# Kernel tuning notes

Hardware: AMD Instinct MI355X
Metric: run time of the kernel (lower is better)

Reference implementation:

```python
import jax, jax.numpy as jnp
import numpy as np

B, S, D, E = 8, 2048, 1024, 8


def setup_inputs() -> dict:
    key = jax.random.key(0)
    k1, k2, k3, k4 = jax.random.split(key, 4)
    return {
        "x": jax.random.normal(k1, (B, S, D), dtype=jnp.float32),
        "routing_scores": jax.random.normal(k2, (B, E), dtype=jnp.float32),
        "expert_w": jax.random.normal(k3, (E, D, D), dtype=jnp.float32) / np.sqrt(D),
        "expert_b": jax.random.normal(k4, (E, D), dtype=jnp.float32),
        "k": 2,
    }


def reference(x, routing_scores, expert_w, expert_b, k):
    batch = routing_scores.shape[0]
    # top-k gating mask + renormalization scale (torch.topk + scatter_ equivalent)
    values, indices = jax.lax.top_k(routing_scores, k)              # (B, k)
    mask = jnp.zeros_like(routing_scores, dtype=bool)
    mask = mask.at[jnp.arange(batch)[:, None], indices].set(True)    # (B, E)
    scale = 1.0 / (values.sum(axis=1, keepdims=True) + 1e-8)         # (B, 1)
    masked_scores = scale * routing_scores * mask                    # (B, E)

    # dense per-expert transform: expert_e(x) = x @ W_e + b_e  -> (E, B, S, D)
    expert_out = jnp.einsum("bsd,edf->ebsf", x, expert_w) + expert_b[:, None, None, :]
    # weighted scatter-accumulate over experts (zero weight for inactive pairs)
    final_output = jnp.einsum("be,ebsf->bsf", masked_scores, expert_out)

    return final_output, mask.sum(axis=0)
```

## Files before the change

### kernel.cpp

```cpp
#include <hip/hip_runtime.h>

#define NB 8
#define NS 2048
#define ND 1024
#define NE 8

typedef unsigned short ushort_t;
typedef __attribute__((ext_vector_type(8))) short bf16x8;
typedef __attribute__((ext_vector_type(4))) float f32x4;

__device__ __forceinline__ unsigned short f2bf(float f) {
    union { float f; unsigned int u; } x; x.f = f;
    unsigned int u = x.u + 0x7fffu + ((x.u >> 16) & 1u);
    return (unsigned short)(u >> 16);
}

__device__ __forceinline__ unsigned pk2(float a, float b) {
    return (unsigned)f2bf(a) | ((unsigned)f2bf(b) << 16);
}

__device__ __forceinline__ void gload16(const void* g, void* l) {
    __builtin_amdgcn_global_load_lds(
        (const __attribute__((address_space(1))) unsigned int*)g,
        (__attribute__((address_space(3))) unsigned int*)l, 16, 0, 0);
}

__device__ __forceinline__ void coef_local(const float* __restrict__ scores,
                                           int b, int k, float* cf) {
    float s[NE];
#pragma unroll
    for (int e = 0; e < NE; ++e) s[e] = scores[b * NE + e];
    bool sel[NE];
#pragma unroll
    for (int e = 0; e < NE; ++e) sel[e] = false;
    float sum = 0.f;
    for (int j = 0; j < k; ++j) {
        int best = 0; float bv = -3.4e38f;
#pragma unroll
        for (int e = 0; e < NE; ++e)
            if (!sel[e] && s[e] > bv) { bv = s[e]; best = e; }
        sel[best] = true; sum += bv;
    }
    float scale = 1.f / (sum + 1e-8f);
#pragma unroll
    for (int e = 0; e < NE; ++e) cf[e] = sel[e] ? scale * s[e] : 0.f;
}

__global__ void prep_kernel(const float* __restrict__ scores,
                            const float* __restrict__ W,
                            const float* __restrict__ eb,
                            const int* __restrict__ kp,
                            ushort_t* __restrict__ wct,
                            float* __restrict__ bias,
                            float* __restrict__ counts) {
    __shared__ float tile[64][65];
    __shared__ int selS[NB][NE];
    int bid = blockIdx.x;
    int t = threadIdx.x;

    if (bid < 2048) {
        int b = bid >> 8;
        int f0 = (bid & 15) * 64, d0 = ((bid >> 4) & 15) * 64;
        float cf[NE];
        coef_local(scores, b, kp[0], cf);
        int lr = t >> 4;
        int lc = (t & 15) * 4;
        float4 acc[4];
#pragma unroll
        for (int it = 0; it < 4; ++it) acc[it] = make_float4(0.f, 0.f, 0.f, 0.f);
#pragma unroll
        for (int e = 0; e < NE; ++e) {
            float c = cf[e];
            if (c != 0.f) {
                const float* We = W + ((size_t)e * ND * ND);
#pragma unroll
                for (int it = 0; it < 4; ++it) {
                    int d = d0 + lr + it * 16;
                    float4 v = *(const float4*)(We + (size_t)d * ND + f0 + lc);
                    acc[it].x += c * v.x; acc[it].y += c * v.y;
                    acc[it].z += c * v.z; acc[it].w += c * v.w;
                }
            }
        }
#pragma unroll
        for (int it = 0; it < 4; ++it) {
            int r = lr + it * 16;
            tile[r][lc + 0] = acc[it].x; tile[r][lc + 1] = acc[it].y;
            tile[r][lc + 2] = acc[it].z; tile[r][lc + 3] = acc[it].w;
        }
        __syncthreads();
        int dl = t & 63;
        int frow = t >> 6;
        ushort_t* dst = wct + (size_t)b * ND * ND + (size_t)f0 * ND + d0 + dl;
#pragma unroll
        for (int it = 0; it < 16; ++it) {
            int f = frow + it * 4;
            dst[(size_t)f * ND] = f2bf(tile[dl][f]);
        }
    } else if (bid < 2080) {
        int i = bid - 2048;
        int b = i >> 2, f = (i & 3) * 256 + t;
        float cf[NE];
        coef_local(scores, b, kp[0], cf);
        float acc = 0.f;
#pragma unroll
        for (int e = 0; e < NE; ++e)
            if (cf[e] != 0.f) acc += cf[e] * eb[e * ND + f];
        bias[b * ND + f] = acc;
    } else {
        int k = kp[0];
        if (t < NB) {
            float s[NE];
#pragma unroll
            for (int e = 0; e < NE; ++e) s[e] = scores[t * NE + e];
            bool sel[NE];
#pragma unroll
            for (int e = 0; e < NE; ++e) sel[e] = false;
            for (int j = 0; j < k; ++j) {
                int best = 0; float bv = -3.4e38f;
#pragma unroll
                for (int e = 0; e < NE; ++e)
                    if (!sel[e] && s[e] > bv) { bv = s[e]; best = e; }
                sel[best] = true;
            }
#pragma unroll
            for (int e = 0; e < NE; ++e) selS[t][e] = sel[e] ? 1 : 0;
        }
        __syncthreads();
        if (t < NE) {
            int c = 0;
#pragma unroll
            for (int b = 0; b < NB; ++b) c += selS[b][t];
            counts[t] = (float)c;
        }
    }
}

__global__ __launch_bounds__(512, 4) void gemm_kernel(const float* __restrict__ x,
                                                      const ushort_t* __restrict__ wct,
                                                      const float* __restrict__ bias,
                                                      float* __restrict__ out) {
    __shared__ ushort_t ldsA[3][256 * 32];
    __shared__ ushort_t ldsB[3][128 * 32];

    int bid = blockIdx.x;
    int b = bid & 7;
    int tile = bid >> 3;
    int m0 = (tile >> 3) * 256;
    int n0 = (tile & 7) * 128;
    const ushort_t* Bt = wct + ((size_t)b * ND * ND) + (size_t)n0 * ND;

    int t = threadIdx.x, lane = t & 63, wave = t >> 6;
    int wm = wave >> 1, wn = wave & 1;
    int fr = lane & 15, fq = lane >> 4;

    int srow = t >> 2;
    int slotg = (t & 3) ^ ((srow >> 1) & 3);
    const ushort_t* sB = Bt + (size_t)srow * ND + slotg * 8;
    int ldstB = t * 8;

    int ar = t >> 1, ah = t & 1;
    const float* xA = x + ((size_t)b * NS * ND) + (size_t)(m0 + ar) * ND + ah * 16;
    int swA = (ar >> 1) & 3;
    int woff0 = ar * 32 + ((2 * ah) ^ swA) * 8;
    int woff1 = ar * 32 + ((2 * ah + 1) ^ swA) * 8;

    int swzb = (fq ^ ((fr >> 1) & 3)) * 16;
    int aoff[4], boff[4];
#pragma unroll
    for (int mi = 0; mi < 4; ++mi) aoff[mi] = (wm * 64 + mi * 16 + fr) * 64 + swzb;
#pragma unroll
    for (int nj = 0; nj < 4; ++nj) boff[nj] = (wn * 64 + nj * 16 + fr) * 64 + swzb;

    f32x4 acc[4][4];
#pragma unroll
    for (int i = 0; i < 4; ++i)
#pragma unroll
        for (int j = 0; j < 4; ++j) acc[i][j] = (f32x4){0.f, 0.f, 0.f, 0.f};

    const int NT = ND / 32;

    float4 rA0, rA1, rA2, rA3;
#define LOAD_A(kt) do { \
    const float* xp = xA + (kt) * 32; \
    rA0 = *(const float4*)(xp);      rA1 = *(const float4*)(xp + 4); \
    rA2 = *(const float4*)(xp + 8);  rA3 = *(const float4*)(xp + 12); \
} while (0)
#define CVT_WRITE(buf) do { \
    uint4 o0, o1; \
    o0.x = pk2(rA0.x, rA0.y); o0.y = pk2(rA0.z, rA0.w); \
    o0.z = pk2(rA1.x, rA1.y); o0.w = pk2(rA1.z, rA1.w); \
    o1.x = pk2(rA2.x, rA2.y); o1.y = pk2(rA2.z, rA2.w); \
    o1.z = pk2(rA3.x, rA3.y); o1.w = pk2(rA3.z, rA3.w); \
    *(uint4*)(&ldsA[buf][woff0]) = o0; \
    *(uint4*)(&ldsA[buf][woff1]) = o1; \
} while (0)

    LOAD_A(0);
    gload16(sB, &ldsB[0][ldstB]);
    gload16(sB + 32, &ldsB[1][ldstB]);
    asm volatile("s_waitcnt vmcnt(2)" ::: "memory");
    CVT_WRITE(0);
    LOAD_A(1);
    asm volatile("s_waitcnt vmcnt(5)" ::: "memory");
    asm volatile("s_waitcnt lgkmcnt(0)" ::: "memory");
    __builtin_amdgcn_s_barrier();

    for (int kt = 0; kt < NT; ++kt) {
        int cur = kt; while (cur >= 3) cur -= 3;
        const char* lA = (const char*)&ldsA[cur][0];
        const char* lB = (const char*)&ldsB[cur][0];
        int nb = cur + 1; if (nb == 3) nb = 0;
        int sq = cur + 2; if (sq >= 3) sq -= 3;

        if (kt + 2 < NT) gload16(sB + (kt + 2) * 32, &ldsB[sq][ldstB]);

        bf16x8 af[4], bf[4];
#pragma unroll
        for (int nj = 0; nj < 4; ++nj) bf[nj] = *(const bf16x8*)(lB + boff[nj]);
#pragma unroll
        for (int mi = 0; mi < 4; ++mi) af[mi] = *(const bf16x8*)(lA + aoff[mi]);
        __builtin_amdgcn_sched_barrier(0);
        asm volatile("s_waitcnt lgkmcnt(0)" ::: "memory");
        __builtin_amdgcn_sched_barrier(0);
        __builtin_amdgcn_s_setprio(1);
#pragma unroll
        for (int mi = 0; mi < 4; ++mi)
#pragma unroll
            for (int nj = 0; nj < 4; ++nj)
                acc[mi][nj] = __builtin_amdgcn_mfma_f32_16x16x32_bf16(af[mi], bf[nj], acc[mi][nj], 0, 0, 0);
        __builtin_amdgcn_s_setprio(0);
        __builtin_amdgcn_sched_barrier(0);

        if (kt + 1 < NT) {
            if (kt + 2 < NT) asm volatile("s_waitcnt vmcnt(1)" ::: "memory");
            else             asm volatile("s_waitcnt vmcnt(0)" ::: "memory");
            __builtin_amdgcn_sched_barrier(0);
            CVT_WRITE(nb);
            if (kt + 2 < NT) LOAD_A(kt + 2);
            __builtin_amdgcn_sched_barrier(0);
            asm volatile("s_waitcnt lgkmcnt(0)" ::: "memory");
            __builtin_amdgcn_s_barrier();
        }
    }

#undef LOAD_A
#undef CVT_WRITE

    const float* bs = bias + b * ND;
    float* O = out + ((size_t)b * NS * ND);
#pragma unroll
    for (int mi = 0; mi < 4; ++mi) {
        int row = m0 + wm * 64 + mi * 16 + fq * 4;
#pragma unroll
        for (int nj = 0; nj < 4; ++nj) {
            int col = n0 + wn * 64 + nj * 16 + fr;
            float bv = bs[col];
            f32x4 v = acc[mi][nj];
#pragma unroll
            for (int r = 0; r < 4; ++r)
                O[(size_t)(row + r) * ND + col] = v[r] + bv;
        }
    }
}

extern "C" void kernel_launch(void* const* d_in, const int* in_sizes, int n_in,
                              void* d_out, int out_size, void* d_ws, size_t ws_size,
                              hipStream_t stream) {
    const float* x      = (const float*)d_in[0];
    const float* scores = (const float*)d_in[1];
    const float* Wx     = (const float*)d_in[2];
    const float* eb     = (const float*)d_in[3];
    const int*   kp     = (const int*)d_in[4];
    float* out = (float*)d_out;
    char* ws = (char*)d_ws;

    float*    bias  = (float*)(ws + 1024);
    ushort_t* wct   = (ushort_t*)(ws + 65536);
    float*    counts = out + (size_t)NB * NS * ND;

    prep_kernel<<<2081, 256, 0, stream>>>(scores, Wx, eb, kp, wct, bias, counts);
    gemm_kernel<<<512, 512, 0, stream>>>(x, wct, bias, out);
}
```

Measured before the change: 74.31 us.

## Split GEMM into producer/consumer waves with smaller 128x128 tiles

After: 126.2 us. 69.9% more time.

```diff
diff --git a/kernel.cpp b/kernel.cpp
--- a/kernel.cpp
+++ b/kernel.cpp
@@ -136,131 +136,133 @@
     }
 }
 
-__global__ __launch_bounds__(512, 4) void gemm_kernel(const float* __restrict__ x,
+__global__ __launch_bounds__(384, 4) void gemm_kernel(const float* __restrict__ x,
                                                       const ushort_t* __restrict__ wct,
                                                       const float* __restrict__ bias,
                                                       float* __restrict__ out) {
-    __shared__ ushort_t ldsA[3][256 * 32];
-    __shared__ ushort_t ldsB[3][128 * 32];
+    __shared__ ushort_t lA[2][128 * 32];
+    __shared__ ushort_t lB[2][128 * 32];
 
     int bid = blockIdx.x;
     int b = bid & 7;
     int tile = bid >> 3;
-    int m0 = (tile >> 3) * 256;
+    int m0 = (tile >> 3) * 128;
     int n0 = (tile & 7) * 128;
-    const ushort_t* Bt = wct + ((size_t)b * ND * ND) + (size_t)n0 * ND;
 
     int t = threadIdx.x, lane = t & 63, wave = t >> 6;
-    int wm = wave >> 1, wn = wave & 1;
-    int fr = lane & 15, fq = lane >> 4;
-
-    int srow = t >> 2;
-    int slotg = (t & 3) ^ ((srow >> 1) & 3);
-    const ushort_t* sB = Bt + (size_t)srow * ND + slotg * 8;
-    int ldstB = t * 8;
-
-    int ar = t >> 1, ah = t & 1;
-    const float* xA = x + ((size_t)b * NS * ND) + (size_t)(m0 + ar) * ND + ah * 16;
-    int swA = (ar >> 1) & 3;
-    int woff0 = ar * 32 + ((2 * ah) ^ swA) * 8;
-    int woff1 = ar * 32 + ((2 * ah + 1) ^ swA) * 8;
-
-    int swzb = (fq ^ ((fr >> 1) & 3)) * 16;
-    int aoff[4], boff[4];
-#pragma unroll
-    for (int mi = 0; mi < 4; ++mi) aoff[mi] = (wm * 64 + mi * 16 + fr) * 64 + swzb;
-#pragma unroll
-    for (int nj = 0; nj < 4; ++nj) boff[nj] = (wn * 64 + nj * 16 + fr) * 64 + swzb;
-
-    f32x4 acc[4][4];
-#pragma unroll
-    for (int i = 0; i < 4; ++i)
-#pragma unroll
-        for (int j = 0; j < 4; ++j) acc[i][j] = (f32x4){0.f, 0.f, 0.f, 0.f};
-
     const int NT = ND / 32;
 
-    float4 rA0, rA1, rA2, rA3;
-#define LOAD_A(kt) do { \
-    const float* xp = xA + (kt) * 32; \
-    rA0 = *(const float4*)(xp);      rA1 = *(const float4*)(xp + 4); \
-    rA2 = *(const float4*)(xp + 8);  rA3 = *(const float4*)(xp + 12); \
+    if (wave < 4) {
+        int wm = wave >> 1, wn = wave & 1;
+        int fr = lane & 15, fq = lane >> 4;
+        int swzb = (fq ^ ((fr >> 1) & 3)) * 16;
+        int aoff[4], boff[4];
+#pragma unroll
+        for (int mi = 0; mi < 4; ++mi) aoff[mi] = (wm * 64 + mi * 16 + fr) * 64 + swzb;
+#pragma unroll
+        for (int nj = 0; nj < 4; ++nj) boff[nj] = (wn * 64 + nj * 16 + fr) * 64 + swzb;
+
+        f32x4 acc[4][4];
+#pragma unroll
+        for (int i = 0; i < 4; ++i)
+#pragma unroll
+            for (int j = 0; j < 4; ++j) acc[i][j] = (f32x4){0.f, 0.f, 0.f, 0.f};
+
+        asm volatile("" ::: "memory");
+        __builtin_amdgcn_s_barrier();
+        asm volatile("" ::: "memory");
+
+        for (int kt = 0; kt < NT; ++kt) {
+            const char* pA = (const char*)&lA[kt & 1][0];
+            const char* pB = (const char*)&lB[kt & 1][0];
+            bf16x8 af[4], bf[4];
+#pragma unroll
+            for (int nj = 0; nj < 4; ++nj) bf[nj] = *(const bf16x8*)(pB + boff[nj]);
+#pragma unroll
+            for (int mi = 0; mi < 4; ++mi) af[mi] = *(const bf16x8*)(pA + aoff[mi]);
+            __builtin_amdgcn_s_setprio(1);
+#pragma unroll
+            for (int mi = 0; mi < 4; ++mi)
+#pragma unroll
+                for (int nj = 0; nj < 4; ++nj)
+                    acc[mi][nj] = __builtin_amdgcn_mfma_f32_16x16x32_bf16(af[mi], bf[nj], acc[mi][nj], 0, 0, 0);
+            __builtin_amdgcn_s_setprio(0);
+            if (kt + 1 < NT) {
+                asm volatile("s_waitcnt lgkmcnt(0)" ::: "memory");
+                __builtin_amdgcn_s_barrier();
+                asm volatile("" ::: "memory");
+            }
+        }
+
+        const float* bs = bias + b * ND;
+        float* O = out + ((size_t)b * NS * ND);
+#pragma unroll
+        for (int mi = 0; mi < 4; ++mi) {
+            int row = m0 + wm * 64 + mi * 16 + fq * 4;
+#pragma unroll
+            for (int nj = 0; nj < 4; ++nj) {
+                int col = n0 + wn * 64 + nj * 16 + fr;
+                float bv = bs[col];
+                f32x4 v = acc[mi][nj];
+#pragma unroll
+                for (int r = 0; r < 4; ++r)
+                    O[(size_t)(row + r) * ND + col] = v[r] + bv;
+            }
+        }
+    } else {
+        int p = t - 256;
+        int pw = wave - 4;
+        const float* xA = x + (size_t)b * NS * ND + (size_t)(m0 + p) * ND;
+        int wsw = (p >> 1) & 3;
+        int brow = pw * 64 + (lane >> 2);
+        int slotB = (lane & 3) ^ ((lane >> 3) & 3);
+        const ushort_t* sB = wct + (size_t)b * ND * ND + (size_t)(n0 + brow) * ND + slotB * 8;
+
+        float4 r[8];
+#define LOADA(kt) do { \
+    const float4* xp = (const float4*)(xA + (kt) * 32); \
+    _Pragma("unroll") \
+    for (int j = 0; j < 8; ++j) r[j] = xp[j]; \
 } while (0)
-#define CVT_WRITE(buf) do { \
-    uint4 o0, o1; \
-    o0.x = pk2(rA0.x, rA0.y); o0.y = pk2(rA0.z, rA0.w); \
-    o0.z = pk2(rA1.x, rA1.y); o0.w = pk2(rA1.z, rA1.w); \
-    o1.x = pk2(rA2.x, rA2.y); o1.y = pk2(rA2.z, rA2.w); \
-    o1.z = pk2(rA3.x, rA3.y); o1.w = pk2(rA3.z, rA3.w); \
-    *(uint4*)(&ldsA[buf][woff0]) = o0; \
-    *(uint4*)(&ldsA[buf][woff1]) = o1; \
+#define GLB(kt, buf) do { \
+    _Pragma("unroll") \
+    for (int i = 0; i < 4; ++i) \
+        gload16(sB + (kt) * 32 + (size_t)(i * 16) * ND, &lB[buf][(pw * 64 + i * 16) * 32]); \
 } while (0)
-
-    LOAD_A(0);
-    gload16(sB, &ldsB[0][ldstB]);
-    gload16(sB + 32, &ldsB[1][ldstB]);
-    asm volatile("s_waitcnt vmcnt(2)" ::: "memory");
-    CVT_WRITE(0);
-    LOAD_A(1);
-    asm volatile("s_waitcnt vmcnt(5)" ::: "memory");
-    asm volatile("s_waitcnt lgkmcnt(0)" ::: "memory");
-    __builtin_amdgcn_s_barrier();
-
-    for (int kt = 0; kt < NT; ++kt) {
-        int cur = kt; while (cur >= 3) cur -= 3;
-        const char* lA = (const char*)&ldsA[cur][0];
-        const char* lB = (const char*)&ldsB[cur][0];
-        int nb = cur + 1; if (nb == 3) nb = 0;
-        int sq = cur + 2; if (sq >= 3) sq -= 3;
-
-        if (kt + 2 < NT) gload16(sB + (kt + 2) * 32, &ldsB[sq][ldstB]);
-
-        bf16x8 af[4], bf[4];
-#pragma unroll
-        for (int nj = 0; nj < 4; ++nj) bf[nj] = *(const bf16x8*)(lB + boff[nj]);
-#pragma unroll
-        for (int mi = 0; mi < 4; ++mi) af[mi] = *(const bf16x8*)(lA + aoff[mi]);
-        __builtin_amdgcn_sched_barrier(0);
+#define CVTW(buf) do { \
+    _Pragma("unroll") \
+    for (int j = 0; j < 4; ++j) { \
+        uint4 o; \
+        o.x = pk2(r[2 * j].x, r[2 * j].y);         o.y = pk2(r[2 * j].z, r[2 * j].w); \
+        o.z = pk2(r[2 * j + 1].x, r[2 * j + 1].y); o.w = pk2(r[2 * j + 1].z, r[2 * j + 1].w); \
+        *(uint4*)(&lA[buf][p * 32 + ((j ^ wsw) * 8)]) = o; \
+    } \
+} while (0)
+
+        LOADA(0);
+        GLB(0, 0);
+        asm volatile("s_waitcnt vmcnt(4)" ::: "memory");
+        CVTW(0);
+        asm volatile("s_waitcnt vmcnt(0)" ::: "memory");
         asm volatile("s_waitcnt lgkmcnt(0)" ::: "memory");
-        __builtin_amdgcn_sched_barrier(0);
-        __builtin_amdgcn_s_setprio(1);
-#pragma unroll
-        for (int mi = 0; mi < 4; ++mi)
-#pragma unroll
-            for (int nj = 0; nj < 4; ++nj)
-                acc[mi][nj] = __builtin_amdgcn_mfma_f32_16x16x32_bf16(af[mi], bf[nj], acc[mi][nj], 0, 0, 0);
-        __builtin_amdgcn_s_setprio(0);
-        __builtin_amdgcn_sched_barrier(0);
-
-        if (kt + 1 < NT) {
-            if (kt + 2 < NT) asm volatile("s_waitcnt vmcnt(1)" ::: "memory");
-            else             asm volatile("s_waitcnt vmcnt(0)" ::: "memory");
-            __builtin_amdgcn_sched_barrier(0);
-            CVT_WRITE(nb);
-            if (kt + 2 < NT) LOAD_A(kt + 2);
-            __builtin_amdgcn_sched_barrier(0);
-            asm volatile("s_waitcnt lgkmcnt(0)" ::: "memory");
-            __builtin_amdgcn_s_barrier();
-        }
-    }
-
-#undef LOAD_A
-#undef CVT_WRITE
-
-    const float* bs = bias + b * ND;
-    float* O = out + ((size_t)b * NS * ND);
-#pragma unroll
-    for (int mi = 0; mi < 4; ++mi) {
-        int row = m0 + wm * 64 + mi * 16 + fq * 4;
-#pragma unroll
-        for (int nj = 0; nj < 4; ++nj) {
-            int col = n0 + wn * 64 + nj * 16 + fr;
-            float bv = bs[col];
-            f32x4 v = acc[mi][nj];
-#pragma unroll
-            for (int r = 0; r < 4; ++r)
-                O[(size_t)(row + r) * ND + col] = v[r] + bv;
-        }
+        LOADA(1);
+        __builtin_amdgcn_s_barrier();
+
+        for (int kt = 0; kt < NT; ++kt) {
+            if (kt + 1 < NT) {
+                int nb = (kt + 1) & 1;
+                GLB(kt + 1, nb);
+                asm volatile("s_waitcnt vmcnt(4)" ::: "memory");
+                CVTW(nb);
+                asm volatile("s_waitcnt vmcnt(0)" ::: "memory");
+                asm volatile("s_waitcnt lgkmcnt(0)" ::: "memory");
+                if (kt + 2 < NT) LOADA(kt + 2);
+                __builtin_amdgcn_s_barrier();
+            }
+        }
+#undef LOADA
+#undef GLB
+#undef CVTW
     }
 }
 
@@ -280,5 +282,5 @@
     float*    counts = out + (size_t)NB * NS * ND;
 
     prep_kernel<<<2081, 256, 0, stream>>>(scores, Wx, eb, kp, wct, bias, counts);
-    gemm_kernel<<<512, 512, 0, stream>>>(x, wct, bias, out);
-}
+    gemm_kernel<<<1024, 384, 0, stream>>>(x, wct, bias, out);
+}
```
